# Kernel tuning notes

Hardware: AMD Instinct MI355X
Metric: run time of the kernel (lower is better)

The kernel has to match this reference:

```python
import jax, jax.numpy as jnp
import numpy as np

B, NKV, NQ, D, H = 4, 2048, 1024, 1024, 16
HD = D // H


def setup_inputs() -> dict:
    key = jax.random.key(0)
    ks = jax.random.split(key, 9)
    s = 0.02
    return {
        "x": jax.random.normal(ks[0], (B, NKV, D), jnp.float32),
        "y": jax.random.normal(ks[1], (B, NQ, D), jnp.float32),
        "mask": jax.random.randint(ks[2], (B, NQ, NKV), 0, 2, jnp.int32),
        "W_kv": jax.random.normal(ks[3], (D, 2 * D), jnp.float32) * s,
        "b_kv": jnp.zeros((2 * D,), jnp.float32),
        "W_q": jax.random.normal(ks[4], (D, D), jnp.float32) * s,
        "b_q": jnp.zeros((D,), jnp.float32),
        "W_o": jax.random.normal(ks[5], (D, D), jnp.float32) * s,
        "b_o": jnp.zeros((D,), jnp.float32),
    }


def reference(x, y, mask, W_kv, b_kv, W_q, b_q, W_o, b_o):
    b, nkv, _ = x.shape
    nq = y.shape[1]
    kv = x @ W_kv + b_kv                                  # [B, NKV, 2D]
    q = y @ W_q + b_q                                     # [B, NQ, D]
    kv = kv.reshape(b, nkv, H, 2 * HD).transpose(0, 2, 1, 3)  # [B,H,NKV,2HD]
    q = q.reshape(b, nq, H, HD).transpose(0, 2, 1, 3)         # [B,H,NQ,HD]
    k, v = kv[..., :HD], kv[..., HD:]
    scores = jnp.einsum('bhqd,bhkd->bhqk', q, k) / jnp.sqrt(jnp.float32(HD))
    scores = jnp.where(mask[:, None, :, :] == 0, jnp.float32(-1e20), scores)
    attn = jax.nn.softmax(scores, axis=-1)
    vals = jnp.einsum('bhqk,bhkd->bhqd', attn, v)          # [B,H,NQ,HD]
    vals = vals.transpose(0, 2, 1, 3).reshape(b, nq, D)
    return vals @ W_o + b_o
```

## Files before the change

kernel.cpp:

```cpp
#include <hip/hip_runtime.h>
#include <hip/hip_bf16.h>
#include <math.h>

#define B_   4
#define NKV_ 2048
#define NQ_  1024
#define D_   1024
#define H_   16
#define HD_  64

typedef __attribute__((ext_vector_type(8))) short bf16x8;
typedef __attribute__((ext_vector_type(4))) float f32x4;

#define MFMA16x32(a, b, c) __builtin_amdgcn_mfma_f32_16x16x32_bf16((a), (b), (c), 0, 0, 0)

#define SC_LOG2 0.1803368801111244f

__device__ __forceinline__ short f2bf(float f) {
    unsigned u = __builtin_bit_cast(unsigned, f);
    u = (u + 0x7fff + ((u >> 16) & 1)) >> 16;
    return (short)u;
}
__device__ __forceinline__ unsigned cvt_pk_bf16(float lo, float hi) {
    unsigned r;
    asm("v_cvt_pk_bf16_f32 %0, %1, %2" : "=v"(r) : "v"(lo), "v"(hi));
    return r;
}
__device__ __forceinline__ void gload_lds16(const void* g, void* l) {
    __builtin_amdgcn_global_load_lds(
        (const __attribute__((address_space(1))) void*)g,
        (__attribute__((address_space(3))) void*)l, 16, 0, 0);
}

__global__ __launch_bounds__(256)
void prep(const float* __restrict__ Wkv, short* __restrict__ Tkv,
          const float* __restrict__ Wq,  short* __restrict__ Tq,
          const float* __restrict__ Wo,  short* __restrict__ To,
          const int* __restrict__ mask,  unsigned short* __restrict__ m16,
          const float* __restrict__ x,   short* __restrict__ xh, int n4x,
          const float* __restrict__ y,   short* __restrict__ yh, int n4y)
{
    const int bid = (int)blockIdx.x;
    if (bid < 4096) {
        const float* W; short* T; int K, N, bx, by;
        if (bid < 2048)      { W = Wkv; T = Tkv; K = D_; N = 2 * D_; bx = bid & 63;          by = bid >> 6; }
        else if (bid < 3072) { W = Wq;  T = Tq;  K = D_; N = D_;     bx = (bid - 2048) & 31; by = (bid - 2048) >> 5; }
        else                 { W = Wo;  T = To;  K = D_; N = D_;     bx = (bid - 3072) & 31; by = (bid - 3072) >> 5; }
        __shared__ float tile[32][33];
        const int tx = threadIdx.x & 31, ty = threadIdx.x >> 5;
        const int n0 = bx * 32, k0 = by * 32;
#pragma unroll
        for (int i = 0; i < 4; ++i)
            tile[ty + 8 * i][tx] = W[(size_t)(k0 + ty + 8 * i) * N + n0 + tx];
        __syncthreads();
#pragma unroll
        for (int i = 0; i < 4; ++i)
            T[(size_t)(n0 + ty + 8 * i) * K + k0 + tx] = f2bf(tile[tx][ty + 8 * i]);
    } else if (bid < 4608) {
        const int w = (bid - 4096) * 256 + threadIdx.x;
        const int4* pp = reinterpret_cast<const int4*>(mask + (size_t)w * 64);
        unsigned wg0 = 0, wg1 = 0, wg2 = 0, wg3 = 0;
#pragma unroll
        for (int i = 0; i < 16; ++i) {
            const int4 v = pp[i];
            const unsigned nib = (unsigned)(v.x != 0) | ((unsigned)(v.y != 0) << 1)
                               | ((unsigned)(v.z != 0) << 2) | ((unsigned)(v.w != 0) << 3);
            const unsigned sh = 4u * (unsigned)(i >> 2);
            if ((i & 3) == 0) wg0 |= nib << sh;
            else if ((i & 3) == 1) wg1 |= nib << sh;
            else if ((i & 3) == 2) wg2 |= nib << sh;
            else wg3 |= nib << sh;
        }
        ushort4 o;
        o.x = (unsigned short)wg0; o.y = (unsigned short)wg1;
        o.z = (unsigned short)wg2; o.w = (unsigned short)wg3;
        reinterpret_cast<ushort4*>(m16)[w] = o;
    } else {
        const int ntot = n4x + n4y;
        for (int i = (bid - 4608) * 256 + threadIdx.x; i < ntot; i += 2048 * 256) {
            const float4 v = (i < n4x)
                ? reinterpret_cast<const float4*>(x)[i]
                : reinterpret_cast<const float4*>(y)[i - n4x];
            short4 h;
            h.x = f2bf(v.x); h.y = f2bf(v.y); h.z = f2bf(v.z); h.w = f2bf(v.w);
            if (i < n4x) reinterpret_cast<short4*>(xh)[i] = h;
            else         reinterpret_cast<short4*>(yh)[i - n4x] = h;
        }
    }
}

__device__ __forceinline__
void gemm_body(int mode, int bidl,
               const short* __restrict__ Ahi, const short* __restrict__ Bhi,
               const float* __restrict__ bias, void* __restrict__ out0,
               void* __restrict__ out1, int M, int N, int K)
{
    __shared__ short At[2][4096];
    __shared__ short Bt[2][4096];

    const int t    = threadIdx.x;
    const int wave = t >> 6;
    const int lane = t & 63;
    const int fr   = lane & 15;
    const int kq   = lane >> 4;

    const int gx  = N >> 7;
    const int gy  = M >> 7;
    const int lgx = __builtin_ctz(gx);
    const int xcd = bidl & 7;
    const int j   = bidl >> 3;
    const int m0  = (xcd * (gy >> 3) + (j >> lgx)) * 128;
    const int n0  = (j & (gx - 1)) * 128;

    const int wm0 = (wave & 1) * 64;
    const int wn0 = (wave >> 1) * 64;
    const int NT  = K >> 5;

    const int r1 = t >> 2,         g1 = (t & 3) ^ ((r1 >> 1) & 3);
    const int r2 = (t + 256) >> 2, g2 = (t & 3) ^ ((r2 >> 1) & 3);

    f32x4 acc[4][4];
#pragma unroll
    for (int i = 0; i < 4; ++i)
#pragma unroll
        for (int j2 = 0; j2 < 4; ++j2) acc[i][j2] = f32x4{0.f, 0.f, 0.f, 0.f};

    auto stage = [&](int nb, int it) {
        const int kk = it << 5;
        gload_lds16(Ahi + (size_t)(m0 + r1) * K + kk + 8 * g1, &At[nb][wave * 512]);
        gload_lds16(Ahi + (size_t)(m0 + r2) * K + kk + 8 * g2, &At[nb][2048 + wave * 512]);
        gload_lds16(Bhi + (size_t)(n0 + r1) * K + kk + 8 * g1, &Bt[nb][wave * 512]);
        gload_lds16(Bhi + (size_t)(n0 + r2) * K + kk + 8 * g2, &Bt[nb][2048 + wave * 512]);
    };

    stage(0, 0);
    asm volatile("s_waitcnt vmcnt(0)" ::: "memory");
    __syncthreads();

    const int gsw = ((kq ^ ((fr >> 1) & 3)) << 3);
    int cur = 0;
    for (int it = 0; it < NT; ++it) {
        if (it + 1 < NT) stage(cur ^ 1, it + 1);
        bf16x8 af[4], bf[4];
#pragma unroll
        for (int i = 0; i < 4; ++i) {
            af[i] = *reinterpret_cast<const bf16x8*>(&At[cur][(wm0 + i * 16 + fr) * 32 + gsw]);
            bf[i] = *reinterpret_cast<const bf16x8*>(&Bt[cur][(wn0 + i * 16 + fr) * 32 + gsw]);
        }
        __builtin_amdgcn_s_setprio(1);
#pragma unroll
        for (int i = 0; i < 4; ++i)
#pragma unroll
            for (int j2 = 0; j2 < 4; ++j2)
                acc[i][j2] = MFMA16x32(af[i], bf[j2], acc[i][j2]);
        __builtin_amdgcn_s_setprio(0);
        asm volatile("s_waitcnt vmcnt(0)" ::: "memory");
        __syncthreads();
        cur ^= 1;
    }

#pragma unroll
    for (int i = 0; i < 4; ++i) {
#pragma unroll
        for (int j2 = 0; j2 < 4; ++j2) {
#pragma unroll
            for (int r = 0; r < 4; ++r) {
                const int m = m0 + wm0 + i * 16 + (lane >> 4) * 4 + r;
                const int n = n0 + wn0 + j2 * 16 + fr;
                const float v = acc[i][j2][r] + bias[n];
                if (mode == 0) {
                    short* K_ = (short*)out0;
                    short* Vt = (short*)out1;
                    const int b  = m >> 11;
                    const int nk = m & 2047;
                    const int h  = n >> 7;
                    const int c  = n & 127;
                    const int bh = b * H_ + h;
                    if (c < 64)
                        K_[(((size_t)bh * NKV_ + nk) << 6) + c] = f2bf(v);
                    else
                        Vt[((size_t)bh * 64 + (c - 64)) * NKV_ + nk] = f2bf(v);
                } else if (mode == 1) {
                    short* Q_ = (short*)out0;
                    const int b = m >> 10;
                    const int q = m & 1023;
                    const int h = n >> 6;
                    const int d = n & 63;
                    Q_[(((size_t)(b * H_ + h) * NQ_ + q) << 6) + d] =
                        f2bf(v * SC_LOG2);
                } else {
                    ((float*)out0)[(size_t)m * N + n] = v;
                }
            }
        }
    }
}

__global__ __launch_bounds__(256)
void proj(const short* __restrict__ xhi, const short* __restrict__ Wkvt,
          const float* __restrict__ b_kv, short* __restrict__ Kbf,
          short* __restrict__ Vtbf,
          const short* __restrict__ yhi, const short* __restrict__ Wqt,
          const float* __restrict__ b_q, short* __restrict__ Qbf)
{
    const int bid = (int)blockIdx.x;
    if (bid < 1024)
        gemm_body(0, bid, xhi, Wkvt, b_kv, Kbf, Vtbf, B_ * NKV_, 2 * D_, D_);
    else
        gemm_body(1, bid - 1024, yhi, Wqt, b_q, Qbf, nullptr, B_ * NQ_, D_, D_);
}

__global__ __launch_bounds__(256)
void ogemm(const short* __restrict__ vals, const short* __restrict__ Wot,
           const float* __restrict__ b_o, float* __restrict__ out)
{
    gemm_body(2, (int)blockIdx.x, vals, Wot, b_o, out, nullptr, B_ * NQ_, D_, D_);
}

__global__ __launch_bounds__(512)
void attn_mfma(const short* __restrict__ Q, const short* __restrict__ K,
               const short* __restrict__ Vt,
               const unsigned short* __restrict__ m16,
               float* __restrict__ Opart, float* __restrict__ Lpart)
{
    __shared__ short KtL[2][4096];
    __shared__ short VtL[2][4096];
    __shared__ short PsL[8192];

    const int t    = threadIdx.x;
    const int wave = t >> 6;
    const int lane = t & 63;
    const int fr   = lane & 15;
    const int g    = lane >> 4;

    const int bid  = (int)blockIdx.x;
    const int xcd  = bid & 7;
    const int j    = bid >> 3;
    const int bh   = xcd * 8 + (j >> 4);
    const int rest = j & 15;
    const int half = rest & 1;
    const int b    = bh >> 4;
    const int h    = bh & 15;
    const int wq0  = (rest >> 1) * 128 + wave * 16;

    const int kts = half * 16;
    const int kte = kts + 16;

    const short* Kg  = K  + (size_t)bh * NKV_ * 64;
    const short* Vtg = Vt + (size_t)bh * 64 * NKV_;

    bf16x8 qf0, qf1;
    {
        const short* Qg = Q + ((size_t)bh * NQ_ + wq0 + fr) * 64 + g * 8;
        qf0 = *reinterpret_cast<const bf16x8*>(Qg);
        qf1 = *reinterpret_cast<const bf16x8*>(Qg + 32);
    }

    bf16x8 ones;
#pragma unroll
    for (int i = 0; i < 8; ++i) ones[i] = (short)0x3F80;

    f32x4 acc_o[4];
#pragma unroll
    for (int n = 0; n < 4; ++n) acc_o[n] = f32x4{0.f, 0.f, 0.f, 0.f};
    f32x4 lacc = f32x4{0.f, 0.f, 0.f, 0.f};

    const unsigned short* mbp =
        m16 + ((size_t)b * NQ_ + wq0 + fr) * (NKV_ / 64) * 4 + g;

    const int r8   = lane >> 3;
    const int csw  = ((lane & 7) << 3) ^ (r8 << 3);
    const int swzf = (fr & 7) << 3;
    short* PsW = PsL + wave * (16 * 64);

    auto stage = [&](int nb, int kt0) {
        const short* sK = Kg + (size_t)(kt0 + wave * 8 + r8) * 64 + csw;
        gload_lds16(sK, &KtL[nb][(wave * 8) * 64]);
        const short* sV = Vtg + (size_t)(wave * 8 + r8) * NKV_ + kt0 + csw;
        gload_lds16(sV, &VtL[nb][(wave * 8) * 64]);
    };

    stage(0, kts * 64);
    asm volatile("s_waitcnt vmcnt(0)" ::: "memory");
    __syncthreads();

    const int kcol0 = (8 * g) ^ swzf;
    const int kcol1 = (32 + 8 * g) ^ swzf;

    int cur = 0;
    for (int kt = kts; kt < kte; ++kt) {
        if (kt + 1 < kte) stage(cur ^ 1, (kt + 1) * 64);

        const unsigned mskv = mbp[(size_t)kt * 4];

        const short* KB = &KtL[cur][fr * 64];
        f32x4 s_acc[4];
        __builtin_amdgcn_s_setprio(1);
#pragma unroll
        for (int t4 = 0; t4 < 4; ++t4) {
            s_acc[t4] = f32x4{0.f, 0.f, 0.f, 0.f};
            const bf16x8 kf0 = *reinterpret_cast<const bf16x8*>(KB + t4 * 1024 + kcol0);
            const bf16x8 kf1 = *reinterpret_cast<const bf16x8*>(KB + t4 * 1024 + kcol1);
            s_acc[t4] = MFMA16x32(kf0, qf0, s_acc[t4]);
            s_acc[t4] = MFMA16x32(kf1, qf1, s_acc[t4]);
        }
        __builtin_amdgcn_s_setprio(0);

        float p[16];
#pragma unroll
        for (int t4 = 0; t4 < 4; ++t4)
#pragma unroll
            for (int r = 0; r < 4; ++r) {
                const int i = 4 * t4 + r;
                const float e = __builtin_amdgcn_exp2f(s_acc[t4][r]);
                p[i] = ((mskv >> i) & 1u) ? e : 0.f;
            }

#pragma unroll
        for (int t4 = 0; t4 < 4; ++t4) {
            uint2 w;
            w.x = cvt_pk_bf16(p[4 * t4 + 0], p[4 * t4 + 1]);
            w.y = cvt_pk_bf16(p[4 * t4 + 2], p[4 * t4 + 3]);
            *reinterpret_cast<uint2*>(&PsW[fr * 64 + ((16 * t4 + 4 * g) ^ swzf)]) = w;
        }

        {
            const bf16x8 pf0 = *reinterpret_cast<const bf16x8*>(&PsW[fr * 64 + kcol0]);
            const bf16x8 pf1 = *reinterpret_cast<const bf16x8*>(&PsW[fr * 64 + kcol1]);
            const short* VB = &VtL[cur][fr * 64];
            __builtin_amdgcn_s_setprio(1);
            lacc = MFMA16x32(ones, pf0, lacc);
            lacc = MFMA16x32(ones, pf1, lacc);
#pragma unroll
            for (int n = 0; n < 4; ++n) {
                const bf16x8 vf0 = *reinterpret_cast<const bf16x8*>(VB + n * 1024 + kcol0);
                const bf16x8 vf1 = *reinterpret_cast<const bf16x8*>(VB + n * 1024 + kcol1);
                acc_o[n] = MFMA16x32(vf0, pf0, acc_o[n]);
                acc_o[n] = MFMA16x32(vf1, pf1, acc_o[n]);
            }
            __builtin_amdgcn_s_setprio(0);
        }

        asm volatile("s_waitcnt vmcnt(0)" ::: "memory");
        __syncthreads();
        cur ^= 1;
    }

    float* Op = Opart + (size_t)half * (B_ * NQ_ * D_);
    const size_t obase = ((size_t)b * NQ_ + wq0 + fr) * D_ + h * 64;
#pragma unroll
    for (int n = 0; n < 4; ++n) {
        float4 v;
        v.x = acc_o[n][0]; v.y = acc_o[n][1];
        v.z = acc_o[n][2]; v.w = acc_o[n][3];
        *reinterpret_cast<float4*>(&Op[obase + 16 * n + 4 * g]) = v;
    }
    if (g == 0)
        Lpart[(size_t)half * (B_ * H_ * NQ_) + (size_t)bh * NQ_ + wq0 + fr] = lacc[0];
}

__global__ __launch_bounds__(256)
void combine(const float* __restrict__ Opart, const float* __restrict__ Lpart,
             short* __restrict__ valshi)
{
    const size_t npart = (size_t)B_ * NQ_ * D_;
    const int n4 = (int)(npart / 4);
    for (int i = blockIdx.x * 256 + threadIdx.x; i < n4; i += 2048 * 256) {
        const int row  = i >> 8;
        const int h    = (i & 255) >> 4;
        const int b    = row >> 10;
        const int q    = row & 1023;
        const float4 o0 = reinterpret_cast<const float4*>(Opart)[i];
        const float4 o1 = reinterpret_cast<const float4*>(Opart + npart)[i];
        const size_t li = (size_t)(b * H_ + h) * NQ_ + q;
        const float inv = 1.f / (Lpart[li] + Lpart[(size_t)B_ * H_ * NQ_ + li]);
        short4 hh;
        hh.x = f2bf((o0.x + o1.x) * inv);
        hh.y = f2bf((o0.y + o1.y) * inv);
        hh.z = f2bf((o0.z + o1.z) * inv);
        hh.w = f2bf((o0.w + o1.w) * inv);
        reinterpret_cast<short4*>(valshi)[i] = hh;
    }
}

extern "C" void kernel_launch(void* const* d_in, const int* in_sizes, int n_in,
                              void* d_out, int out_size, void* d_ws, size_t ws_size,
                              hipStream_t stream)
{
    const float* x    = (const float*)d_in[0];
    const float* y    = (const float*)d_in[1];
    const int*   mask = (const int*)  d_in[2];
    const float* W_kv = (const float*)d_in[3];
    const float* b_kv = (const float*)d_in[4];
    const float* W_q  = (const float*)d_in[5];
    const float* b_q  = (const float*)d_in[6];
    const float* W_o  = (const float*)d_in[7];
    const float* b_o  = (const float*)d_in[8];
    float* out = (float*)d_out;

    char* p = (char*)d_ws;
    auto take = [&](size_t bytes) { char* r = p; p += bytes; return r; };
    short* xhi    = (short*)take((size_t)B_ * NKV_ * D_ * 2);
    short* yhi    = (short*)take((size_t)B_ * NQ_ * D_ * 2);
    short* Wkvthi = (short*)take((size_t)2 * D_ * D_ * 2);
    short* Wqthi  = (short*)take((size_t)D_ * D_ * 2);
    short* Wothi  = (short*)take((size_t)D_ * D_ * 2);
    short* Kbf    = (short*)take((size_t)B_ * H_ * NKV_ * HD_ * 2);
    short* Vtbf   = (short*)take((size_t)B_ * H_ * HD_ * NKV_ * 2);
    short* Qbf    = (short*)take((size_t)B_ * H_ * NQ_ * HD_ * 2);
    unsigned short* m16 =
        (unsigned short*)take((size_t)B_ * NQ_ * (NKV_ / 64) * 4 * 2);
    float* Opart  = (float*)take((size_t)2 * B_ * NQ_ * D_ * 4);
    float* Lpart  = (float*)take((size_t)2 * B_ * H_ * NQ_ * 4);
    short* valshi = xhi;

    prep<<<6656, 256, 0, stream>>>(W_kv, Wkvthi, W_q, Wqthi, W_o, Wothi,
                                   mask, m16,
                                   x, xhi, B_ * NKV_ * D_ / 4,
                                   y, yhi, B_ * NQ_ * D_ / 4);

    proj<<<1280, 256, 0, stream>>>(xhi, Wkvthi, b_kv, Kbf, Vtbf,
                                   yhi, Wqthi, b_q, Qbf);

    attn_mfma<<<1024, 512, 0, stream>>>(Qbf, Kbf, Vtbf, m16, Opart, Lpart);

    combine<<<2048, 256, 0, stream>>>(Opart, Lpart, valshi);

    ogemm<<<256, 256, 0, stream>>>(valshi, Wothi, b_o, out);

    (void)in_sizes; (void)n_in; (void)out_size; (void)ws_size;
}
```

Measured before the change: 189.0 us.

## Triple-buffer GEMM LDS pipeline and split output GEMM into 64-row tiles

The shared GEMM body moves from double to triple buffering. It issues loads two K-steps ahead, waits with a partial vmcnt, and needs only one barrier per iteration instead of a full drain. The output projection becomes a dedicated kernel with 64x128 tiles and 512 blocks, so more CUs have work on the small M=4096 GEMM. Both add LDS usage, and the partial waitcnt counts must exactly match the number of loads issued per stage.

```diff
diff --git a/kernel.cpp b/kernel.cpp
--- a/kernel.cpp
+++ b/kernel.cpp
@@ -30,6 +30,11 @@
     __builtin_amdgcn_global_load_lds(
         (const __attribute__((address_space(1))) void*)g,
         (__attribute__((address_space(3))) void*)l, 16, 0, 0);
+}
+__device__ __forceinline__ void barrier_raw() {
+    asm volatile("" ::: "memory");
+    __builtin_amdgcn_s_barrier();
+    asm volatile("" ::: "memory");
 }
 
 __global__ __launch_bounds__(256)
@@ -95,8 +100,8 @@
                const float* __restrict__ bias, void* __restrict__ out0,
                void* __restrict__ out1, int M, int N, int K)
 {
-    __shared__ short At[2][4096];
-    __shared__ short Bt[2][4096];
+    __shared__ short At[3][4096];
+    __shared__ short Bt[3][4096];
 
     const int t    = threadIdx.x;
     const int wave = t >> 6;
@@ -125,28 +130,32 @@
 #pragma unroll
         for (int j2 = 0; j2 < 4; ++j2) acc[i][j2] = f32x4{0.f, 0.f, 0.f, 0.f};
 
-    auto stage = [&](int nb, int it) {
+    auto stage = [&](int sb, int it) {
         const int kk = it << 5;
-        gload_lds16(Ahi + (size_t)(m0 + r1) * K + kk + 8 * g1, &At[nb][wave * 512]);
-        gload_lds16(Ahi + (size_t)(m0 + r2) * K + kk + 8 * g2, &At[nb][2048 + wave * 512]);
-        gload_lds16(Bhi + (size_t)(n0 + r1) * K + kk + 8 * g1, &Bt[nb][wave * 512]);
-        gload_lds16(Bhi + (size_t)(n0 + r2) * K + kk + 8 * g2, &Bt[nb][2048 + wave * 512]);
+        gload_lds16(Ahi + (size_t)(m0 + r1) * K + kk + 8 * g1, &At[sb][wave * 512]);
+        gload_lds16(Ahi + (size_t)(m0 + r2) * K + kk + 8 * g2, &At[sb][2048 + wave * 512]);
+        gload_lds16(Bhi + (size_t)(n0 + r1) * K + kk + 8 * g1, &Bt[sb][wave * 512]);
+        gload_lds16(Bhi + (size_t)(n0 + r2) * K + kk + 8 * g2, &Bt[sb][2048 + wave * 512]);
     };
 
     stage(0, 0);
-    asm volatile("s_waitcnt vmcnt(0)" ::: "memory");
-    __syncthreads();
+    if (NT > 1) stage(1, 1);
 
     const int gsw = ((kq ^ ((fr >> 1) & 3)) << 3);
-    int cur = 0;
     for (int it = 0; it < NT; ++it) {
-        if (it + 1 < NT) stage(cur ^ 1, it + 1);
+        if (it + 1 < NT) asm volatile("s_waitcnt vmcnt(4)" ::: "memory");
+        else             asm volatile("s_waitcnt vmcnt(0)" ::: "memory");
+        barrier_raw();
+
+        const int cb = it % 3;
         bf16x8 af[4], bf[4];
 #pragma unroll
         for (int i = 0; i < 4; ++i) {
-            af[i] = *reinterpret_cast<const bf16x8*>(&At[cur][(wm0 + i * 16 + fr) * 32 + gsw]);
-            bf[i] = *reinterpret_cast<const bf16x8*>(&Bt[cur][(wn0 + i * 16 + fr) * 32 + gsw]);
-        }
+            af[i] = *reinterpret_cast<const bf16x8*>(&At[cb][(wm0 + i * 16 + fr) * 32 + gsw]);
+            bf[i] = *reinterpret_cast<const bf16x8*>(&Bt[cb][(wn0 + i * 16 + fr) * 32 + gsw]);
+        }
+        if (it + 2 < NT) stage((it + 2) % 3, it + 2);
+
         __builtin_amdgcn_s_setprio(1);
 #pragma unroll
         for (int i = 0; i < 4; ++i)
@@ -154,9 +163,6 @@
             for (int j2 = 0; j2 < 4; ++j2)
                 acc[i][j2] = MFMA16x32(af[i], bf[j2], acc[i][j2]);
         __builtin_amdgcn_s_setprio(0);
-        asm volatile("s_waitcnt vmcnt(0)" ::: "memory");
-        __syncthreads();
-        cur ^= 1;
     }
 
 #pragma unroll
@@ -211,10 +217,87 @@
 }
 
 __global__ __launch_bounds__(256)
-void ogemm(const short* __restrict__ vals, const short* __restrict__ Wot,
-           const float* __restrict__ b_o, float* __restrict__ out)
-{
-    gemm_body(2, (int)blockIdx.x, vals, Wot, b_o, out, nullptr, B_ * NQ_, D_, D_);
+void ogemm(const short* __restrict__ Ahi, const short* __restrict__ Bhi,
+           const float* __restrict__ bias, float* __restrict__ out)
+{
+    __shared__ short At[3][2048];
+    __shared__ short Bt[3][4096];
+
+    const int M = B_ * NQ_, N = D_, K = D_;
+    const int t    = threadIdx.x;
+    const int wave = t >> 6;
+    const int lane = t & 63;
+    const int fr   = lane & 15;
+    const int kq   = lane >> 4;
+
+    const int gx  = N >> 7;
+    const int gy  = M >> 6;
+    const int lgx = __builtin_ctz(gx);
+    const int bid = (int)blockIdx.x;
+    const int xcd = bid & 7;
+    const int j   = bid >> 3;
+    const int m0  = (xcd * (gy >> 3) + (j >> lgx)) * 64;
+    const int n0  = (j & (gx - 1)) * 128;
+
+    const int wm0 = (wave & 1) * 32;
+    const int wn0 = (wave >> 1) * 64;
+    const int NT  = K >> 5;
+
+    const int rA = t >> 2, gA = (t & 3) ^ ((rA >> 1) & 3);
+    const int r1 = t >> 2,         g1 = (t & 3) ^ ((r1 >> 1) & 3);
+    const int r2 = (t + 256) >> 2, g2 = (t & 3) ^ ((r2 >> 1) & 3);
+
+    f32x4 acc[2][4];
+#pragma unroll
+    for (int i = 0; i < 2; ++i)
+#pragma unroll
+        for (int j2 = 0; j2 < 4; ++j2) acc[i][j2] = f32x4{0.f, 0.f, 0.f, 0.f};
+
+    auto stage = [&](int sb, int it) {
+        const int kk = it << 5;
+        gload_lds16(Ahi + (size_t)(m0 + rA) * K + kk + 8 * gA, &At[sb][wave * 512]);
+        gload_lds16(Bhi + (size_t)(n0 + r1) * K + kk + 8 * g1, &Bt[sb][wave * 512]);
+        gload_lds16(Bhi + (size_t)(n0 + r2) * K + kk + 8 * g2, &Bt[sb][2048 + wave * 512]);
+    };
+
+    stage(0, 0);
+    if (NT > 1) stage(1, 1);
+
+    const int gsw = ((kq ^ ((fr >> 1) & 3)) << 3);
+    for (int it = 0; it < NT; ++it) {
+        if (it + 1 < NT) asm volatile("s_waitcnt vmcnt(3)" ::: "memory");
+        else             asm volatile("s_waitcnt vmcnt(0)" ::: "memory");
+        barrier_raw();
+
+        const int cb = it % 3;
+        bf16x8 af[2], bf[4];
+#pragma unroll
+        for (int i = 0; i < 2; ++i)
+            af[i] = *reinterpret_cast<const bf16x8*>(&At[cb][(wm0 + i * 16 + fr) * 32 + gsw]);
+#pragma unroll
+        for (int i = 0; i < 4; ++i)
+            bf[i] = *reinterpret_cast<const bf16x8*>(&Bt[cb][(wn0 + i * 16 + fr) * 32 + gsw]);
+        if (it + 2 < NT) stage((it + 2) % 3, it + 2);
+
+        __builtin_amdgcn_s_setprio(1);
+#pragma unroll
+        for (int i = 0; i < 2; ++i)
+#pragma unroll
+            for (int j2 = 0; j2 < 4; ++j2)
+                acc[i][j2] = MFMA16x32(af[i], bf[j2], acc[i][j2]);
+        __builtin_amdgcn_s_setprio(0);
+    }
+
+#pragma unroll
+    for (int i = 0; i < 2; ++i)
+#pragma unroll
+        for (int j2 = 0; j2 < 4; ++j2)
+#pragma unroll
+            for (int r = 0; r < 4; ++r) {
+                const int m = m0 + wm0 + i * 16 + (lane >> 4) * 4 + r;
+                const int n = n0 + wn0 + j2 * 16 + fr;
+                out[(size_t)m * N + n] = acc[i][j2][r] + bias[n];
+            }
 }
 
 __global__ __launch_bounds__(512)
@@ -426,7 +509,7 @@
 
     combine<<<2048, 256, 0, stream>>>(Opart, Lpart, valshi);
 
-    ogemm<<<256, 256, 0, stream>>>(valshi, Wothi, b_o, out);
+    ogemm<<<512, 256, 0, stream>>>(valshi, Wothi, b_o, out);
 
     (void)in_sizes; (void)n_in; (void)out_size; (void)ws_size;
 }
```

Result: faster. 182.4 us (-3.5%).
